# Performance work log

Hardware: AMD Instinct MI355X
Metric: run time of the kernel (lower is better)

## Reference

```python
import math
import jax, jax.numpy as jnp
import numpy as np

B = 4096
IN_FEATURES = 512
OUT_FEATURES = 1024
SPARSITY = 0.01  # kwta.sparsity
X_DENSITY = 0.1  # fraction of active bits in the binary SDR input


def setup_inputs() -> dict:
    key = jax.random.key(0)
    kx, kw = jax.random.split(key)
    # binary sparse SDR input (the module counts nonzeros, expects sparse binary x)
    x = (jax.random.uniform(kx, (B, IN_FEATURES)) < X_DENSITY).astype(jnp.float32)
    weight = jax.random.normal(kw, (OUT_FEATURES, IN_FEATURES), dtype=jnp.float32)
    return {"x": x, "weight": weight}


def reference(x, weight):
    Bn, in_f = x.shape
    out_f = weight.shape[0]
    k_active = math.ceil(SPARSITY * out_f)   # serial MP steps (11)
    k_in = math.ceil(SPARSITY * in_f)        # kwta winners on xr (6)
    rows = jnp.arange(Bn)

    nonzero = jnp.sum(x != 0, axis=1)
    lambd = (3 * jnp.max(nonzero) * in_f).astype(jnp.float32)

    def wta(r):  # one-hot argmax per row -> binary [B, out_f]
        idx = jnp.argmax(r, axis=1)
        return jnp.zeros_like(r).at[rows, idx].set(1.0)

    def kwta(v):  # binary top-k per row -> binary [B, in_f]
        _, idx = jax.lax.top_k(v, k_in)
        return jnp.zeros_like(v).at[rows[:, None], idx].set(1.0)

    two_x = 2.0 * x
    wT = weight.T  # [in_f, out_f]

    def step(carry, _):
        encoded, xr = carry
        residual = (two_x - xr) @ wT - lambd * encoded      # [B, out_f]
        encoded = encoded + wta(residual)
        xr = kwta(encoded @ weight)                          # [B, in_f]
        return (encoded, xr), None

    init = (jnp.zeros((Bn, out_f), jnp.float32), jnp.zeros_like(x))
    (encoded, xr), _ = jax.lax.scan(step, init, None, length=k_active)
    return encoded, xr
```

## Files before the change

### kernel.cpp

```cpp
#include <hip/hip_runtime.h>

#define IN_F 512
#define OUT_F 1024
#define K_ACTIVE 11
#define K_IN 6

__global__ __launch_bounds__(256) void transpose_w_kernel(const float* __restrict__ w,
                                                          float* __restrict__ wT) {
    __shared__ float tile[32][33];
    const int tx = threadIdx.x & 31;
    const int ty = threadIdx.x >> 5;
    const int i0 = blockIdx.x * 32;
    const int j0 = blockIdx.y * 32;
#pragma unroll
    for (int k = 0; k < 4; ++k)
        tile[ty + 8 * k][tx] = w[(size_t)(j0 + ty + 8 * k) * IN_F + (i0 + tx)];
    __syncthreads();
#pragma unroll
    for (int k = 0; k < 4; ++k)
        wT[(size_t)(i0 + ty + 8 * k) * OUT_F + (j0 + tx)] = tile[tx][ty + 8 * k];
}

__device__ __forceinline__ unsigned long long pack_key(double v, unsigned rev,
                                                       unsigned long long mask) {
    unsigned long long b = (unsigned long long)__double_as_longlong(v);
    unsigned long long m =
        (unsigned long long)((long long)b >> 63) | 0x8000000000000000ull;
    unsigned long long u = b ^ m;
    return (u & ~mask) | (unsigned long long)rev;
}

template <int C>
__device__ __forceinline__ unsigned long long dppmax(unsigned long long k) {
    unsigned lo = (unsigned)__builtin_amdgcn_update_dpp(0, (int)(unsigned)k, C, 0xF, 0xF, true);
    unsigned hi = (unsigned)__builtin_amdgcn_update_dpp(0, (int)(unsigned)(k >> 32), C, 0xF, 0xF, true);
    unsigned long long o = ((unsigned long long)hi << 32) | lo;
    return o > k ? o : k;
}

__device__ __forceinline__ unsigned long long wave_max_u64(unsigned long long k) {
    k = dppmax<0x111>(k);
    k = dppmax<0x112>(k);
    k = dppmax<0x114>(k);
    k = dppmax<0x118>(k);
    k = dppmax<0x142>(k);
    k = dppmax<0x143>(k);
    unsigned glo = (unsigned)__builtin_amdgcn_readlane((int)(unsigned)k, 63);
    unsigned ghi = (unsigned)__builtin_amdgcn_readlane((int)(unsigned)(k >> 32), 63);
    return ((unsigned long long)ghi << 32) | glo;
}

template <bool USE_T>
__device__ __forceinline__ void wt_row_axpy(double* r, const float* __restrict__ wT,
                                            const float* __restrict__ w, int i,
                                            double sgn, int lane, int wv) {
    if constexpr (USE_T) {
        const float* rp = wT + ((size_t)i << 10) + (wv << 9) + (lane << 2);
#pragma unroll
        for (int c = 0; c < 2; ++c) {
            const float4 f = *(const float4*)(rp + (c << 8));
            r[4 * c + 0] += sgn * (double)f.x;
            r[4 * c + 1] += sgn * (double)f.y;
            r[4 * c + 2] += sgn * (double)f.z;
            r[4 * c + 3] += sgn * (double)f.w;
        }
    } else {
#pragma unroll
        for (int s = 0; s < 8; ++s) {
            int j = (wv << 9) | ((s >> 2) << 8) | (lane << 2) | (s & 3);
            r[s] += sgn * (double)w[(size_t)j * IN_F + i];
        }
    }
}

template <bool USE_T>
__global__ __launch_bounds__(128) void bmp_kernel(const float* __restrict__ x,
                                                  const float* __restrict__ w,
                                                  const float* __restrict__ wT,
                                                  float* __restrict__ out, int rows) {
    __shared__ unsigned short act[IN_F + 8];
    __shared__ unsigned long long kx[4];
    const int lane = threadIdx.x & 63;
    const int wv = threadIdx.x >> 6;
    const int row = blockIdx.x;
    if (row >= rows) return;

    const float* xrow = x + (size_t)row * IN_F;
    int cnt = 0;
#pragma unroll
    for (int c = 0; c < IN_F / 64; ++c) {
        bool pbit = xrow[c * 64 + lane] != 0.0f;
        unsigned long long m = __ballot(pbit);
        int pre = __popcll(m & ((1ull << lane) - 1ull));
        if (wv == 0 && pbit) act[cnt + pre] = (unsigned short)(c * 64 + lane);
        cnt += __popcll(m);
    }
    __syncthreads();

    int rc = 0;
    auto block_max = [&](unsigned long long k) -> unsigned long long {
        const unsigned long long wm = wave_max_u64(k);
        if (lane == 0) kx[((rc & 1) << 1) | wv] = wm;
        __syncthreads();
        const unsigned long long a = kx[(rc & 1) << 1];
        const unsigned long long b = kx[((rc & 1) << 1) | 1];
        ++rc;
        return a > b ? a : b;
    };

    double r[8];
#pragma unroll
    for (int s = 0; s < 8; ++s) r[s] = 0.0;
    {
        int iu = act[0];
#pragma unroll 1
        for (int k = 0; k < cnt; ++k) {
            int inx = act[k + 1];
            wt_row_axpy<USE_T>(r, wT, w, iu, 1.0, lane, wv);
            iu = inx;
        }
    }
#pragma unroll
    for (int s = 0; s < 8; ++s) r[s] *= 2.0;

    double vd[4];
#pragma unroll
    for (int p = 0; p < 4; ++p) vd[p] = 0.0;

    unsigned enc = 0;
    unsigned selmask = 0;
    int O0 = -1, O1 = -1, O2 = -1, O3 = -1, O4 = -1, O5 = -1;

#pragma unroll 1
    for (int t = 0; t < K_ACTIVE; ++t) {
        unsigned long long kb = 0;
#pragma unroll
        for (int s = 0; s < 8; ++s) {
            int j = (wv << 9) | ((s >> 2) << 8) | (lane << 2) | (s & 3);
            unsigned long long key = pack_key(r[s], 1023u ^ (unsigned)j, 1023ull);
            key = (enc & (1u << s)) ? 0ull : key;
            kb = key > kb ? key : kb;
        }
        const unsigned long long g = block_max(kb);
        const int bestj =
            __builtin_amdgcn_readfirstlane(1023 ^ (int)(g & 1023ull));
        if ((bestj >> 9) == wv && ((bestj >> 2) & 63) == lane)
            enc |= 1u << ((((bestj >> 8) & 1) << 2) | (bestj & 3));

        {
            const float* wr = w + ((size_t)bestj << 9) + (wv << 8) + (lane << 2);
            const float4 f = *(const float4*)wr;
            vd[0] += (double)f.x;
            vd[1] += (double)f.y;
            vd[2] += (double)f.z;
            vd[3] += (double)f.w;
        }

        int N[6];
        {
            unsigned long long vkey[4];
#pragma unroll
            for (int p = 0; p < 4; ++p) {
                int i = (wv << 8) | (lane << 2) | p;
                vkey[p] = pack_key(vd[p], 511u ^ (unsigned)i, 511ull);
            }
#pragma unroll
            for (int s2 = 0; s2 < K_IN; ++s2) {
                unsigned long long lk = vkey[0];
#pragma unroll
                for (int p = 1; p < 4; ++p) lk = vkey[p] > lk ? vkey[p] : lk;
                const unsigned long long gk = block_max(lk);
                N[s2] = __builtin_amdgcn_readfirstlane(511 ^ (int)(gk & 511ull));
#pragma unroll
                for (int p = 0; p < 4; ++p) vkey[p] = (vkey[p] == gk) ? 0ull : vkey[p];
            }
            if (t == K_ACTIVE - 1) {
                selmask = 0;
#pragma unroll
                for (int p = 0; p < 4; ++p) selmask |= (vkey[p] == 0ull) ? (1u << p) : 0u;
            }
        }

        if (t == 0) {
#pragma unroll
            for (int b = 0; b < 6; ++b) wt_row_axpy<USE_T>(r, wT, w, N[b], -1.0, lane, wv);
        } else if (t < K_ACTIVE - 1) {
#pragma unroll
            for (int a = 0; a < 6; ++a) {
                const int o = (a == 0) ? O0 : (a == 1) ? O1 : (a == 2) ? O2
                              : (a == 3) ? O3 : (a == 4) ? O4 : O5;
                const bool stay = (o == N[0]) | (o == N[1]) | (o == N[2]) |
                                  (o == N[3]) | (o == N[4]) | (o == N[5]);
                if (!stay) wt_row_axpy<USE_T>(r, wT, w, o, 1.0, lane, wv);
            }
#pragma unroll
            for (int b = 0; b < 6; ++b) {
                const int n = N[b];
                const bool was = (n == O0) | (n == O1) | (n == O2) |
                                 (n == O3) | (n == O4) | (n == O5);
                if (!was) wt_row_axpy<USE_T>(r, wT, w, n, -1.0, lane, wv);
            }
        }
        O0 = N[0]; O1 = N[1]; O2 = N[2]; O3 = N[3]; O4 = N[4]; O5 = N[5];
    }

    float* oe = out + (size_t)row * OUT_F + (wv << 9) + (lane << 2);
#pragma unroll
    for (int c = 0; c < 2; ++c) {
        float4 v;
        v.x = (enc & (1u << (4 * c + 0))) ? 1.0f : 0.0f;
        v.y = (enc & (1u << (4 * c + 1))) ? 1.0f : 0.0f;
        v.z = (enc & (1u << (4 * c + 2))) ? 1.0f : 0.0f;
        v.w = (enc & (1u << (4 * c + 3))) ? 1.0f : 0.0f;
        *(float4*)(oe + (c << 8)) = v;
    }
    float* ox = out + (size_t)rows * OUT_F + (size_t)row * IN_F + (wv << 8) + (lane << 2);
    {
        float4 v;
        v.x = (selmask & 1u) ? 1.0f : 0.0f;
        v.y = (selmask & 2u) ? 1.0f : 0.0f;
        v.z = (selmask & 4u) ? 1.0f : 0.0f;
        v.w = (selmask & 8u) ? 1.0f : 0.0f;
        *(float4*)ox = v;
    }
}

extern "C" void kernel_launch(void* const* d_in, const int* in_sizes, int n_in,
                              void* d_out, int out_size, void* d_ws, size_t ws_size,
                              hipStream_t stream) {
    const float* x = (const float*)d_in[0];
    const float* w = (const float*)d_in[1];
    float* out = (float*)d_out;
    const int rows = in_sizes[0] / IN_F;

    const size_t wt_bytes = (size_t)IN_F * OUT_F * sizeof(float);
    if (ws_size >= wt_bytes && d_ws != nullptr) {
        float* wT = (float*)d_ws;
        transpose_w_kernel<<<dim3(IN_F / 32, OUT_F / 32), 256, 0, stream>>>(w, wT);
        bmp_kernel<true><<<rows, 128, 0, stream>>>(x, w, wT, out, rows);
    } else {
        bmp_kernel<false><<<rows, 128, 0, stream>>>(x, w, nullptr, out, rows);
    }
}
```

Measured before the change: 170.4 us.

## Pre-convert transposed weights to double and pair row gathers with a zero pad row

Adds a transpose kernel that writes the weight transpose as doubles plus a zero sentinel row, so the per-row axpy loads doubles directly instead of converting floats. The initial x·Wᵀ accumulation processes two active input indices per iteration, using the zero row to pad odd counts. The wave max reduction is changed to reduce the high 32 bits first and resolve the low bits only on ties. This doubles the weight bytes gathered per row and needs a larger workspace, in exchange for fewer conversions and less DPP work.

```diff
diff --git a/kernel.cpp b/kernel.cpp
--- a/kernel.cpp
+++ b/kernel.cpp
@@ -4,6 +4,25 @@
 #define OUT_F 1024
 #define K_ACTIVE 11
 #define K_IN 6
+
+__global__ __launch_bounds__(256) void transpose_wd_kernel(const float* __restrict__ w,
+                                                           double* __restrict__ wTd) {
+    __shared__ float tile[32][33];
+    const int tx = threadIdx.x & 31;
+    const int ty = threadIdx.x >> 5;
+    const int i0 = blockIdx.x * 32;
+    const int j0 = blockIdx.y * 32;
+#pragma unroll
+    for (int k = 0; k < 4; ++k)
+        tile[ty + 8 * k][tx] = w[(size_t)(j0 + ty + 8 * k) * IN_F + (i0 + tx)];
+    __syncthreads();
+#pragma unroll
+    for (int k = 0; k < 4; ++k)
+        wTd[(size_t)(i0 + ty + 8 * k) * OUT_F + (j0 + tx)] = (double)tile[tx][ty + 8 * k];
+}
+__global__ void zero_row_d_kernel(double* __restrict__ wTd) {
+    wTd[(size_t)IN_F * OUT_F + blockIdx.x * 256 + threadIdx.x] = 0.0;
+}
 
 __global__ __launch_bounds__(256) void transpose_w_kernel(const float* __restrict__ w,
                                                           float* __restrict__ wT) {
@@ -20,6 +39,9 @@
     for (int k = 0; k < 4; ++k)
         wT[(size_t)(i0 + ty + 8 * k) * OUT_F + (j0 + tx)] = tile[tx][ty + 8 * k];
 }
+__global__ void zero_row_f_kernel(float* __restrict__ wT) {
+    wT[(size_t)IN_F * OUT_F + blockIdx.x * 256 + threadIdx.x] = 0.0f;
+}
 
 __device__ __forceinline__ unsigned long long pack_key(double v, unsigned rev,
                                                        unsigned long long mask) {
@@ -31,30 +53,51 @@
 }
 
 template <int C>
-__device__ __forceinline__ unsigned long long dppmax(unsigned long long k) {
-    unsigned lo = (unsigned)__builtin_amdgcn_update_dpp(0, (int)(unsigned)k, C, 0xF, 0xF, true);
-    unsigned hi = (unsigned)__builtin_amdgcn_update_dpp(0, (int)(unsigned)(k >> 32), C, 0xF, 0xF, true);
-    unsigned long long o = ((unsigned long long)hi << 32) | lo;
-    return o > k ? o : k;
-}
-
-__device__ __forceinline__ unsigned long long wave_max_u64(unsigned long long k) {
-    k = dppmax<0x111>(k);
-    k = dppmax<0x112>(k);
-    k = dppmax<0x114>(k);
-    k = dppmax<0x118>(k);
-    k = dppmax<0x142>(k);
-    k = dppmax<0x143>(k);
-    unsigned glo = (unsigned)__builtin_amdgcn_readlane((int)(unsigned)k, 63);
-    unsigned ghi = (unsigned)__builtin_amdgcn_readlane((int)(unsigned)(k >> 32), 63);
-    return ((unsigned long long)ghi << 32) | glo;
-}
-
-template <bool USE_T>
-__device__ __forceinline__ void wt_row_axpy(double* r, const float* __restrict__ wT,
-                                            const float* __restrict__ w, int i,
-                                            double sgn, int lane, int wv) {
-    if constexpr (USE_T) {
+__device__ __forceinline__ unsigned maxdpp(unsigned v) {
+    unsigned t = (unsigned)__builtin_amdgcn_update_dpp(0, (int)v, C, 0xF, 0xF, true);
+    return t > v ? t : v;
+}
+__device__ __forceinline__ unsigned wave_umax(unsigned v) {
+    v = maxdpp<0x111>(v);
+    v = maxdpp<0x112>(v);
+    v = maxdpp<0x114>(v);
+    v = maxdpp<0x118>(v);
+    v = maxdpp<0x142>(v);
+    v = maxdpp<0x143>(v);
+    return (unsigned)__builtin_amdgcn_readlane((int)v, 63);
+}
+
+__device__ __forceinline__ unsigned long long wave_max_key(unsigned long long k) {
+    const unsigned h = (unsigned)(k >> 32), l = (unsigned)k;
+    const unsigned gh = wave_umax(h);
+    const unsigned long long tied = __ballot(h == gh);
+    unsigned gl;
+    if (__popcll(tied) == 1) {
+        gl = (unsigned)__builtin_amdgcn_readlane((int)l,
+                                                 (int)__ffsll((long long)tied) - 1);
+    } else {
+        gl = wave_umax((h == gh) ? l : 0u);
+    }
+    return ((unsigned long long)gh << 32) | gl;
+}
+
+template <int MODE>
+__device__ __forceinline__ void row_axpy(double* r, const double* __restrict__ wTd,
+                                         const float* __restrict__ wT,
+                                         const float* __restrict__ w, int i,
+                                         double sgn, int lane, int wv) {
+    if constexpr (MODE == 2) {
+        const double* rp = wTd + ((size_t)i << 10) + (wv << 9) + (lane << 2);
+#pragma unroll
+        for (int c = 0; c < 2; ++c) {
+            const double2 a = *(const double2*)(rp + (c << 8));
+            const double2 b = *(const double2*)(rp + (c << 8) + 2);
+            r[4 * c + 0] += sgn * a.x;
+            r[4 * c + 1] += sgn * a.y;
+            r[4 * c + 2] += sgn * b.x;
+            r[4 * c + 3] += sgn * b.y;
+        }
+    } else if constexpr (MODE == 1) {
         const float* rp = wT + ((size_t)i << 10) + (wv << 9) + (lane << 2);
 #pragma unroll
         for (int c = 0; c < 2; ++c) {
@@ -73,10 +116,44 @@
     }
 }
 
-template <bool USE_T>
+template <int MODE>
+__device__ __forceinline__ void row_add2(double* r, const double* __restrict__ wTd,
+                                         const float* __restrict__ wT, int i0, int i1,
+                                         int lane, int wv) {
+    if constexpr (MODE == 2) {
+        const double* p0 = wTd + ((size_t)i0 << 10) + (wv << 9) + (lane << 2);
+        const double* p1 = wTd + ((size_t)i1 << 10) + (wv << 9) + (lane << 2);
+        const double2 a0 = *(const double2*)(p0);
+        const double2 a1 = *(const double2*)(p0 + 2);
+        const double2 a2 = *(const double2*)(p0 + 256);
+        const double2 a3 = *(const double2*)(p0 + 258);
+        const double2 b0 = *(const double2*)(p1);
+        const double2 b1 = *(const double2*)(p1 + 2);
+        const double2 b2 = *(const double2*)(p1 + 256);
+        const double2 b3 = *(const double2*)(p1 + 258);
+        r[0] += a0.x + b0.x;  r[1] += a0.y + b0.y;
+        r[2] += a1.x + b1.x;  r[3] += a1.y + b1.y;
+        r[4] += a2.x + b2.x;  r[5] += a2.y + b2.y;
+        r[6] += a3.x + b3.x;  r[7] += a3.y + b3.y;
+    } else {
+        const float* p0 = wT + ((size_t)i0 << 10) + (wv << 9) + (lane << 2);
+        const float* p1 = wT + ((size_t)i1 << 10) + (wv << 9) + (lane << 2);
+        const float4 f0 = *(const float4*)(p0);
+        const float4 f1 = *(const float4*)(p0 + 256);
+        const float4 g0 = *(const float4*)(p1);
+        const float4 g1 = *(const float4*)(p1 + 256);
+        r[0] += (double)f0.x + (double)g0.x;  r[1] += (double)f0.y + (double)g0.y;
+        r[2] += (double)f0.z + (double)g0.z;  r[3] += (double)f0.w + (double)g0.w;
+        r[4] += (double)f1.x + (double)g1.x;  r[5] += (double)f1.y + (double)g1.y;
+        r[6] += (double)f1.z + (double)g1.z;  r[7] += (double)f1.w + (double)g1.w;
+    }
+}
+
+template <int MODE>
 __global__ __launch_bounds__(128) void bmp_kernel(const float* __restrict__ x,
                                                   const float* __restrict__ w,
                                                   const float* __restrict__ wT,
+                                                  const double* __restrict__ wTd,
                                                   float* __restrict__ out, int rows) {
     __shared__ unsigned short act[IN_F + 8];
     __shared__ unsigned long long kx[4];
@@ -95,11 +172,12 @@
         if (wv == 0 && pbit) act[cnt + pre] = (unsigned short)(c * 64 + lane);
         cnt += __popcll(m);
     }
+    if (wv == 0 && lane < 2) act[cnt + lane] = (unsigned short)IN_F;
     __syncthreads();
 
     int rc = 0;
     auto block_max = [&](unsigned long long k) -> unsigned long long {
-        const unsigned long long wm = wave_max_u64(k);
+        const unsigned long long wm = wave_max_key(k);
         if (lane == 0) kx[((rc & 1) << 1) | wv] = wm;
         __syncthreads();
         const unsigned long long a = kx[(rc & 1) << 1];
@@ -111,14 +189,15 @@
     double r[8];
 #pragma unroll
     for (int s = 0; s < 8; ++s) r[s] = 0.0;
-    {
-        int iu = act[0];
+    if constexpr (MODE >= 1) {
 #pragma unroll 1
-        for (int k = 0; k < cnt; ++k) {
-            int inx = act[k + 1];
-            wt_row_axpy<USE_T>(r, wT, w, iu, 1.0, lane, wv);
-            iu = inx;
-        }
+        for (int k = 0; k < cnt; k += 2) {
+            const int i0 = act[k], i1 = act[k + 1];
+            row_add2<MODE>(r, wTd, wT, i0, i1, lane, wv);
+        }
+    } else {
+#pragma unroll 1
+        for (int k = 0; k < cnt; ++k) row_axpy<0>(r, wTd, wT, w, act[k], 1.0, lane, wv);
     }
 #pragma unroll
     for (int s = 0; s < 8; ++s) r[s] *= 2.0;
@@ -183,7 +262,8 @@
 
         if (t == 0) {
 #pragma unroll
-            for (int b = 0; b < 6; ++b) wt_row_axpy<USE_T>(r, wT, w, N[b], -1.0, lane, wv);
+            for (int b = 0; b < 6; ++b)
+                row_axpy<MODE>(r, wTd, wT, w, N[b], -1.0, lane, wv);
         } else if (t < K_ACTIVE - 1) {
 #pragma unroll
             for (int a = 0; a < 6; ++a) {
@@ -191,14 +271,14 @@
                               : (a == 3) ? O3 : (a == 4) ? O4 : O5;
                 const bool stay = (o == N[0]) | (o == N[1]) | (o == N[2]) |
                                   (o == N[3]) | (o == N[4]) | (o == N[5]);
-                if (!stay) wt_row_axpy<USE_T>(r, wT, w, o, 1.0, lane, wv);
+                if (!stay) row_axpy<MODE>(r, wTd, wT, w, o, 1.0, lane, wv);
             }
 #pragma unroll
             for (int b = 0; b < 6; ++b) {
                 const int n = N[b];
                 const bool was = (n == O0) | (n == O1) | (n == O2) |
                                  (n == O3) | (n == O4) | (n == O5);
-                if (!was) wt_row_axpy<USE_T>(r, wT, w, n, -1.0, lane, wv);
+                if (!was) row_axpy<MODE>(r, wTd, wT, w, n, -1.0, lane, wv);
             }
         }
         O0 = N[0]; O1 = N[1]; O2 = N[2]; O3 = N[3]; O4 = N[4]; O5 = N[5];
@@ -233,12 +313,20 @@
     float* out = (float*)d_out;
     const int rows = in_sizes[0] / IN_F;
 
-    const size_t wt_bytes = (size_t)IN_F * OUT_F * sizeof(float);
-    if (ws_size >= wt_bytes && d_ws != nullptr) {
+    const size_t need_d = (size_t)(IN_F + 1) * OUT_F * sizeof(double);
+    const size_t need_f = (size_t)(IN_F + 1) * OUT_F * sizeof(float);
+
+    if (d_ws != nullptr && ws_size >= need_d) {
+        double* wTd = (double*)d_ws;
+        transpose_wd_kernel<<<dim3(IN_F / 32, OUT_F / 32), 256, 0, stream>>>(w, wTd);
+        zero_row_d_kernel<<<OUT_F / 256, 256, 0, stream>>>(wTd);
+        bmp_kernel<2><<<rows, 128, 0, stream>>>(x, w, nullptr, wTd, out, rows);
+    } else if (d_ws != nullptr && ws_size >= need_f) {
         float* wT = (float*)d_ws;
         transpose_w_kernel<<<dim3(IN_F / 32, OUT_F / 32), 256, 0, stream>>>(w, wT);
-        bmp_kernel<true><<<rows, 128, 0, stream>>>(x, w, wT, out, rows);
-    } else {
-        bmp_kernel<false><<<rows, 128, 0, stream>>>(x, w, nullptr, out, rows);
-    }
-}
+        zero_row_f_kernel<<<OUT_F / 256, 256, 0, stream>>>(wT);
+        bmp_kernel<1><<<rows, 128, 0, stream>>>(x, w, wT, nullptr, out, rows);
+    } else {
+        bmp_kernel<0><<<rows, 128, 0, stream>>>(x, w, nullptr, nullptr, out, rows);
+    }
+}
```

Measured after the change: 204.0 us. 1.2x slower.
